# Performance work log

Measured on AMD Instinct MI355X. Metric: run time of the kernel, lower is better.

## Reference

```python
import jax, jax.numpy as jnp
import numpy as np

IN_C = 512
OUT_C = 1024
N = 8192


def _xavier(key, shape):
    fan_in, fan_out = shape[1], shape[0]
    limit = float(np.sqrt(6.0 / (fan_in + fan_out)))
    return jax.random.uniform(key, shape, jnp.float32, -limit, limit)


def setup_inputs() -> dict:
    key = jax.random.key(0)
    ks = jax.random.split(key, 20)
    inp = {
        'x': jax.random.normal(ks[0], (IN_C, N), jnp.float32),
        'c_prev_dim0': jax.random.normal(ks[1], (OUT_C, N), jnp.float32),
        'h_prev_dim0': jax.random.normal(ks[2], (OUT_C, N), jnp.float32),
        'c_prev_dim1': jax.random.normal(ks[3], (OUT_C, N), jnp.float32),
        'h_prev_dim1': jax.random.normal(ks[4], (OUT_C, N), jnp.float32),
    }
    names_x = ['w_ii', 'w_if', 'w_ig', 'w_io']
    names_h = ['w_hi', 'w_hf', 'w_hg', 'w_ho']
    names_b = ['b_i', 'b_f', 'b_g', 'b_o']
    k = 5
    for n in names_x:
        inp[n] = _xavier(ks[k], (OUT_C, IN_C)); k += 1
    for n in names_h:
        inp[n] = _xavier(ks[k], (OUT_C, OUT_C)); k += 1
    for n in names_b:
        inp[n] = _xavier(ks[k], (OUT_C, 1)); k += 1
    inp['weighted_sum'] = jax.random.uniform(ks[k], (2,), jnp.float32)
    return inp


def reference(x, c_prev_dim0, h_prev_dim0, c_prev_dim1, h_prev_dim1,
              w_ii, w_if, w_ig, w_io,
              w_hi, w_hf, w_hg, w_ho,
              b_i, b_f, b_g, b_o,
              weighted_sum):
    # Input projections shared by both spatial directions: (out, N)
    xi = w_ii @ x
    xf = w_if @ x
    xg = w_ig @ x
    xo = w_io @ x

    def gates(h_prev, c_prev):
        i = jax.nn.sigmoid(xi + w_hi @ h_prev + b_i)
        f = jax.nn.sigmoid(xf + w_hf @ h_prev + b_f)
        g = jnp.tanh(xg + w_hg @ h_prev + b_g)
        o = jax.nn.sigmoid(xo + w_ho @ h_prev + b_o)
        c = f * c_prev + i * g
        h = o * jnp.tanh(c)
        return c, h

    ct0, ht0 = gates(h_prev_dim0, c_prev_dim0)
    ct1, ht1 = gates(h_prev_dim1, c_prev_dim1)
    ct = ct0 * weighted_sum[0] + ct1 * weighted_sum[1]
    ht = ht0 * weighted_sum[0] + ht1 * weighted_sum[1]
    return ct, ht
```

## Files before the change

### kernel.cpp

```cpp
#include <hip/hip_runtime.h>
#include <cstdint>
#include <cstddef>

#define IN_C  512
#define OUT_C 1024
#define NSAMP 8192
#define KTOT  1536

typedef __bf16 bf16x8 __attribute__((ext_vector_type(8)));
typedef float  f32x4  __attribute__((ext_vector_type(4)));

#define SBAR() __builtin_amdgcn_s_barrier()

__device__ __forceinline__ unsigned short f2bf(float f) {
    unsigned int u = __float_as_uint(f);
    u += 0x7FFFu + ((u >> 16) & 1u);
    return (unsigned short)(u >> 16);
}
__device__ __forceinline__ float sigmoid_f(float x) { return 1.0f / (1.0f + __expf(-x)); }
__device__ __forceinline__ float tanh_f(float x) {
    float e = __expf(2.0f * x);
    return 1.0f - 2.0f / (e + 1.0f);
}

__global__ void tcvt_kernel(const float* __restrict__ in, unsigned short* __restrict__ out,
                            int R, int C) {
    __shared__ float t[32][33];
    const int tx = threadIdx.x, ty = threadIdx.y;
    const int c0 = blockIdx.x * 32, r0 = blockIdx.y * 32;
#pragma unroll
    for (int i = 0; i < 4; ++i)
        t[ty + i * 8][tx] = in[(size_t)(r0 + ty + i * 8) * C + (c0 + tx)];
    __syncthreads();
#pragma unroll
    for (int i = 0; i < 4; ++i)
        out[(size_t)(c0 + ty + i * 8) * R + (r0 + tx)] = f2bf(t[tx][ty + i * 8]);
}

__global__ void packA_kernel(const float* __restrict__ x0, const float* __restrict__ x1,
                             const float* __restrict__ x2, const float* __restrict__ x3,
                             const float* __restrict__ h0, const float* __restrict__ h1,
                             const float* __restrict__ h2, const float* __restrict__ h3,
                             unsigned short* __restrict__ Ap) {
    const int idx = blockIdx.x * 256 + threadIdx.x;
    const int m = idx / 192, k8 = idx % 192;
    const int g = m & 3, r = m >> 2;
    const float* src;
    if (k8 < 64) {
        const float* a = (g & 2) ? ((g & 1) ? x3 : x2) : ((g & 1) ? x1 : x0);
        src = a + (size_t)r * IN_C + k8 * 8;
    } else {
        const float* a = (g & 2) ? ((g & 1) ? h3 : h2) : ((g & 1) ? h1 : h0);
        src = a + (size_t)r * OUT_C + (k8 - 64) * 8;
    }
    float4 v0 = reinterpret_cast<const float4*>(src)[0];
    float4 v1 = reinterpret_cast<const float4*>(src)[1];
    ushort4 o0, o1;
    o0.x = f2bf(v0.x); o0.y = f2bf(v0.y); o0.z = f2bf(v0.z); o0.w = f2bf(v0.w);
    o1.x = f2bf(v1.x); o1.y = f2bf(v1.y); o1.z = f2bf(v1.z); o1.w = f2bf(v1.w);
    ushort4* dst = reinterpret_cast<ushort4*>(Ap + (size_t)m * KTOT + k8 * 8);
    dst[0] = o0; dst[1] = o1;
}

__global__ __launch_bounds__(512, 2) void mdlstm_main(
    const unsigned short* __restrict__ Ap,
    const unsigned short* __restrict__ xT,
    const unsigned short* __restrict__ h0T,
    const unsigned short* __restrict__ h1T,
    const float* __restrict__ b_i, const float* __restrict__ b_f,
    const float* __restrict__ b_g, const float* __restrict__ b_o,
    const float* __restrict__ cp0, const float* __restrict__ cp1,
    const float* __restrict__ wsum,
    float* __restrict__ out)
{
    __shared__ __align__(16) unsigned char smem[131072];

    const int tid  = threadIdx.x;
    const int lane = tid & 63;
    const int wid  = tid >> 6;
    const int wm   = wid >> 2;
    const int wn   = wid & 3;
    const int g4   = lane >> 4;
    const int l16  = lane & 15;

    const int by    = blockIdx.y;
    const int bcol  = blockIdx.x * 128;
    const int browM = by * 256;

    f32x4 acc[8][4];
#pragma unroll
    for (int mf = 0; mf < 8; ++mf)
#pragma unroll
        for (int nf = 0; nf < 4; ++nf)
            acc[mf][nf] = (f32x4){0.f, 0.f, 0.f, 0.f};

    auto stage_A = [&](int P, int hA, int j1) {
#pragma unroll
        for (int c = 0; c < 2; ++c) {
            const int u    = c * 8192 + tid * 16;
            const int rloc = (u >> 6) & 127;
            const int kb   = (u & 63) ^ (((u >> 7) & 3) << 4);
            const char* src = (const char*)Ap
                + ((size_t)(browM + hA * 128 + rloc) * KTOT + j1 * 64 + c * 32) * 2 + kb;
            __builtin_amdgcn_global_load_lds((const unsigned int*)src,
                (unsigned int*)(smem + P * 65536 + hA * 16384 + u), 16, 0, 0);
        }
    };
    auto stage_B = [&](int P, int d, int j2) {
#pragma unroll
        for (int c = 0; c < 2; ++c) {
            const int u    = c * 8192 + tid * 16;
            const int rloc = (u >> 6) & 127;
            const int kb   = (u & 63) ^ (((u >> 7) & 3) << 4);
            const char* src;
            if (j2 < 8) {
                src = (const char*)xT + ((size_t)(bcol + rloc) * IN_C + j2 * 64 + c * 32) * 2 + kb;
            } else {
                const unsigned short* hsrc = d ? h1T : h0T;
                src = (const char*)hsrc + ((size_t)(bcol + rloc) * OUT_C + (j2 - 8) * 64 + c * 32) * 2 + kb;
            }
            __builtin_amdgcn_global_load_lds((const unsigned int*)src,
                (unsigned int*)(smem + P * 65536 + 32768 + d * 16384 + u), 16, 0, 0);
        }
    };

    auto swzb = [](int u) { return u ^ (((u >> 7) & 3) << 4); };
    auto fragA = [&](int P, int mf, int kk) -> bf16x8 {
        const int u = kk * 8192 + (mf * 16 + l16) * 64 + g4 * 16;
        return *reinterpret_cast<const bf16x8*>(smem + P * 65536 + wm * 16384 + swzb(u));
    };
    auto fragB = [&](int P, int nf, int kk) -> bf16x8 {
        const int u = kk * 8192 + ((wn & 1) * 64 + nf * 16 + l16) * 64 + g4 * 16;
        return *reinterpret_cast<const bf16x8*>(smem + P * 65536 + 32768 + (wn >> 1) * 16384 + swzb(u));
    };

    auto ktile = [&](int j, int P, int PN, bool stA, bool stB, bool tail) {
        bf16x8 bF[4][2], aF[2][2];
        auto mfma_pair = [&](int M) {
            __builtin_amdgcn_s_setprio(1);
#pragma unroll
            for (int kk = 0; kk < 2; ++kk)
#pragma unroll
                for (int mi = 0; mi < 2; ++mi)
#pragma unroll
                    for (int nf = 0; nf < 4; ++nf)
                        acc[M + mi][nf] = __builtin_amdgcn_mfma_f32_16x16x32_bf16(
                            aF[mi][kk], bF[nf][kk], acc[M + mi][nf], 0, 0, 0);
            __builtin_amdgcn_s_setprio(0);
        };
#pragma unroll
        for (int nf = 0; nf < 4; ++nf) { bF[nf][0] = fragB(P, nf, 0); bF[nf][1] = fragB(P, nf, 1); }
#pragma unroll
        for (int kk = 0; kk < 2; ++kk) { aF[0][kk] = fragA(P, 0, kk); aF[1][kk] = fragA(P, 1, kk); }
        if (stA) stage_A(PN, 0, j + 1);
        SBAR();
        mfma_pair(0);
        SBAR();
#pragma unroll
        for (int kk = 0; kk < 2; ++kk) { aF[0][kk] = fragA(P, 2, kk); aF[1][kk] = fragA(P, 3, kk); }
        if (stA) stage_A(PN, 1, j + 1);
        SBAR();
        mfma_pair(2);
        SBAR();
#pragma unroll
        for (int kk = 0; kk < 2; ++kk) { aF[0][kk] = fragA(P, 4, kk); aF[1][kk] = fragA(P, 5, kk); }
        if (stB) stage_B(P, 0, j + 2);
        SBAR();
        mfma_pair(4);
        SBAR();
#pragma unroll
        for (int kk = 0; kk < 2; ++kk) { aF[0][kk] = fragA(P, 6, kk); aF[1][kk] = fragA(P, 7, kk); }
        if (stB) stage_B(P, 1, j + 2);
        SBAR();
        mfma_pair(6);
        if (!tail) asm volatile("s_waitcnt vmcnt(4)");
        else       asm volatile("s_waitcnt vmcnt(0)");
        SBAR();
    };

    stage_A(0, 0, 0); stage_A(0, 1, 0);
    stage_B(0, 0, 0); stage_B(0, 1, 0);
    stage_B(1, 0, 1); stage_B(1, 1, 1);
    asm volatile("s_waitcnt vmcnt(4)");
    SBAR();

#pragma unroll 1
    for (int jj = 0; jj < 12; ++jj) {
        const bool s = (jj < 11);
        ktile(2 * jj,     0, 1, true, s, !s);
        ktile(2 * jj + 1, 1, 0, s,    s, !s);
    }

    const float w0 = wsum[0], w1 = wsum[1];
    const int   d  = wn >> 1;
    const float* cp = d ? cp1 : cp0;
    const float wd  = d ? w1 : w0;

    float rc[8][4], rh[8][4];
#pragma unroll
    for (int mf = 0; mf < 8; ++mf) {
        const int orow = by * 64 + wm * 32 + mf * 4 + g4;
        const float bi = b_i[orow], bff = b_f[orow], bg = b_g[orow], bo = b_o[orow];
#pragma unroll
        for (int nf = 0; nf < 4; ++nf) {
            const int scol = bcol + (wn & 1) * 64 + nf * 16 + l16;
            float i_ = sigmoid_f(acc[mf][nf][0] + bi);
            float f_ = sigmoid_f(acc[mf][nf][1] + bff);
            float g_ = tanh_f  (acc[mf][nf][2] + bg);
            float o_ = sigmoid_f(acc[mf][nf][3] + bo);
            float cc = f_ * cp[(size_t)orow * NSAMP + scol] + i_ * g_;
            float hh = o_ * tanh_f(cc);
            rc[mf][nf] = wd * cc;
            rh[mf][nf] = wd * hh;
        }
    }

    float* ex = (float*)smem;
    const int rbase = (wm * 2 + (wn & 1)) * 4096;
    if (d == 1) {
#pragma unroll
        for (int mf = 0; mf < 8; ++mf)
#pragma unroll
            for (int nf = 0; nf < 4; ++nf) {
                const int slot = rbase + (mf * 4 + nf) * 64 + lane;
                ex[slot]        = rc[mf][nf];
                ex[slot + 2048] = rh[mf][nf];
            }
    }
    SBAR();
    if (d == 0) {
#pragma unroll
        for (int mf = 0; mf < 8; ++mf) {
            const int orow = by * 64 + wm * 32 + mf * 4 + g4;
#pragma unroll
            for (int nf = 0; nf < 4; ++nf) {
                const int scol = bcol + (wn & 1) * 64 + nf * 16 + l16;
                const int slot = rbase + (mf * 4 + nf) * 64 + lane;
                out[(size_t)orow * NSAMP + scol] = rc[mf][nf] + ex[slot];
                out[(size_t)OUT_C * NSAMP + (size_t)orow * NSAMP + scol] = rh[mf][nf] + ex[slot + 2048];
            }
        }
    }
}

extern "C" void kernel_launch(void* const* d_in, const int* in_sizes, int n_in,
                              void* d_out, int out_size, void* d_ws, size_t ws_size,
                              hipStream_t stream) {
    (void)in_sizes; (void)n_in; (void)out_size; (void)ws_size;

    const float* x    = (const float*)d_in[0];
    const float* cp0  = (const float*)d_in[1];
    const float* hp0  = (const float*)d_in[2];
    const float* cp1  = (const float*)d_in[3];
    const float* hp1  = (const float*)d_in[4];
    const float* b_i  = (const float*)d_in[13];
    const float* b_f  = (const float*)d_in[14];
    const float* b_g  = (const float*)d_in[15];
    const float* b_o  = (const float*)d_in[16];
    const float* wsum = (const float*)d_in[17];
    float* out = (float*)d_out;

    char* ws = (char*)d_ws;
    unsigned short* xT  = (unsigned short*)(ws);
    unsigned short* h0T = (unsigned short*)(ws + (size_t)8  * 1024 * 1024);
    unsigned short* h1T = (unsigned short*)(ws + (size_t)24 * 1024 * 1024);
    unsigned short* Ap  = (unsigned short*)(ws + (size_t)40 * 1024 * 1024);

    dim3 tb(32, 8);
    tcvt_kernel<<<dim3(NSAMP / 32, IN_C  / 32), tb, 0, stream>>>(x,   xT,  IN_C,  NSAMP);
    tcvt_kernel<<<dim3(NSAMP / 32, OUT_C / 32), tb, 0, stream>>>(hp0, h0T, OUT_C, NSAMP);
    tcvt_kernel<<<dim3(NSAMP / 32, OUT_C / 32), tb, 0, stream>>>(hp1, h1T, OUT_C, NSAMP);

    packA_kernel<<<(4096 * 192) / 256, 256, 0, stream>>>(
        (const float*)d_in[5], (const float*)d_in[6], (const float*)d_in[7], (const float*)d_in[8],
        (const float*)d_in[9], (const float*)d_in[10], (const float*)d_in[11], (const float*)d_in[12],
        Ap);

    mdlstm_main<<<dim3(NSAMP / 128, OUT_C / 64), 512, 0, stream>>>(
        Ap, xT, h0T, h1T, b_i, b_f, b_g, b_o, cp0, cp1, wsum, out);
}
```

Measured before the change: 256.2 us.

## Software-pipeline LDS fragment loads across MFMA clusters and drop half the barriers

Restructures the k-tile loop so the A fragments for the next MFMA cluster are read from LDS while the current cluster runs, and the next tile's B and first A fragments are preloaded at the end of each tile. This cuts the barriers per tile from eight to four and adds sched_barrier fences around the vmcnt waits. The aim is to hide LDS read latency behind MFMA work and reduce barrier stalls. It keeps more fragment registers live across barriers, which raises register pressure and requires the wait and barrier ordering to remain correct at the tile boundaries.

```diff
diff --git a/kernel.cpp b/kernel.cpp
--- a/kernel.cpp
+++ b/kernel.cpp
@@ -10,7 +10,10 @@
 typedef __bf16 bf16x8 __attribute__((ext_vector_type(8)));
 typedef float  f32x4  __attribute__((ext_vector_type(4)));
 
-#define SBAR() __builtin_amdgcn_s_barrier()
+#define SBAR()   __builtin_amdgcn_s_barrier()
+#define SFENCE() __builtin_amdgcn_sched_barrier(0)
+#define VM4()    asm volatile("s_waitcnt vmcnt(4)")
+#define VM0()    asm volatile("s_waitcnt vmcnt(0)")
 
 __device__ __forceinline__ unsigned short f2bf(float f) {
     unsigned int u = __float_as_uint(f);
@@ -134,61 +137,66 @@
         return *reinterpret_cast<const bf16x8*>(smem + P * 65536 + 32768 + (wn >> 1) * 16384 + swzb(u));
     };
 
-    auto ktile = [&](int j, int P, int PN, bool stA, bool stB, bool tail) {
-        bf16x8 bF[4][2], aF[2][2];
-        auto mfma_pair = [&](int M) {
-            __builtin_amdgcn_s_setprio(1);
-#pragma unroll
-            for (int kk = 0; kk < 2; ++kk)
-#pragma unroll
-                for (int mi = 0; mi < 2; ++mi)
-#pragma unroll
-                    for (int nf = 0; nf < 4; ++nf)
-                        acc[M + mi][nf] = __builtin_amdgcn_mfma_f32_16x16x32_bf16(
-                            aF[mi][kk], bF[nf][kk], acc[M + mi][nf], 0, 0, 0);
-            __builtin_amdgcn_s_setprio(0);
-        };
-#pragma unroll
-        for (int nf = 0; nf < 4; ++nf) { bF[nf][0] = fragB(P, nf, 0); bF[nf][1] = fragB(P, nf, 1); }
-#pragma unroll
-        for (int kk = 0; kk < 2; ++kk) { aF[0][kk] = fragA(P, 0, kk); aF[1][kk] = fragA(P, 1, kk); }
+    bf16x8 aF[2][2];
+    bf16x8 bF[4][2];
+
+    auto cluster = [&](int M) {
+        __builtin_amdgcn_s_setprio(1);
+#pragma unroll
+        for (int kk = 0; kk < 2; ++kk)
+#pragma unroll
+            for (int mi = 0; mi < 2; ++mi)
+#pragma unroll
+                for (int nf = 0; nf < 4; ++nf)
+                    acc[M + mi][nf] = __builtin_amdgcn_mfma_f32_16x16x32_bf16(
+                        aF[mi][kk], bF[nf][kk], acc[M + mi][nf], 0, 0, 0);
+        __builtin_amdgcn_s_setprio(0);
+    };
+    auto loadA = [&](int P, int mf) {
+#pragma unroll
+        for (int kk = 0; kk < 2; ++kk) { aF[0][kk] = fragA(P, mf, kk); aF[1][kk] = fragA(P, mf + 1, kk); }
+    };
+    auto loadB = [&](int P) {
+#pragma unroll
+        for (int nf = 0; nf < 4; ++nf)
+#pragma unroll
+            for (int kk = 0; kk < 2; ++kk) bF[nf][kk] = fragB(P, nf, kk);
+    };
+
+    auto ktile = [&](int j, int P, int PN) {
+        const bool stA = (j < 23);
+        const bool stB = (j < 22);
+        cluster(0);
+        loadA(P, 2);
         if (stA) stage_A(PN, 0, j + 1);
         SBAR();
-        mfma_pair(0);
-        SBAR();
-#pragma unroll
-        for (int kk = 0; kk < 2; ++kk) { aF[0][kk] = fragA(P, 2, kk); aF[1][kk] = fragA(P, 3, kk); }
+        cluster(2);
+        loadA(P, 4);
         if (stA) stage_A(PN, 1, j + 1);
         SBAR();
-        mfma_pair(2);
-        SBAR();
-#pragma unroll
-        for (int kk = 0; kk < 2; ++kk) { aF[0][kk] = fragA(P, 4, kk); aF[1][kk] = fragA(P, 5, kk); }
+        cluster(4);
+        loadA(P, 6);
         if (stB) stage_B(P, 0, j + 2);
         SBAR();
-        mfma_pair(4);
-        SBAR();
-#pragma unroll
-        for (int kk = 0; kk < 2; ++kk) { aF[0][kk] = fragA(P, 6, kk); aF[1][kk] = fragA(P, 7, kk); }
+        cluster(6);
         if (stB) stage_B(P, 1, j + 2);
-        SBAR();
-        mfma_pair(6);
-        if (!tail) asm volatile("s_waitcnt vmcnt(4)");
-        else       asm volatile("s_waitcnt vmcnt(0)");
+        if (j < 22)       { SFENCE(); VM4(); SFENCE(); }
+        else if (j == 22) { SFENCE(); VM0(); SFENCE(); }
+        if (j < 23) { loadB(PN); loadA(PN, 0); }
         SBAR();
     };
 
     stage_A(0, 0, 0); stage_A(0, 1, 0);
     stage_B(0, 0, 0); stage_B(0, 1, 0);
     stage_B(1, 0, 1); stage_B(1, 1, 1);
-    asm volatile("s_waitcnt vmcnt(4)");
+    SFENCE(); VM4(); SFENCE();
     SBAR();
+    loadB(0); loadA(0, 0);
 
 #pragma unroll 1
     for (int jj = 0; jj < 12; ++jj) {
-        const bool s = (jj < 11);
-        ktile(2 * jj,     0, 1, true, s, !s);
-        ktile(2 * jj + 1, 1, 0, s,    s, !s);
+        ktile(2 * jj,     0, 1);
+        ktile(2 * jj + 1, 1, 0);
     }
 
     const float w0 = wsum[0], w1 = wsum[1];
```

After: 245.7 us. 4.1% less time.
